# Kernel tuning notes

Hardware: AMD Instinct MI355X
Metric: run time of the kernel (lower is better)

## Reference

```python
import jax, jax.numpy as jnp
import numpy as np

N_NODES = 100000
N_EDGES = 1600000


def _spmm(row, col, val, x, n):
    # out[i] = sum_{e: row[e]==i} val[e] * x[col[e]]  (sparse adj @ dense x)
    return jax.ops.segment_sum(val[:, None] * x[col], row, num_segments=n)


def setup_inputs() -> dict:
    key = jax.random.key(0)
    ks = jax.random.split(key, 6)
    x = jax.random.normal(ks[0], (N_NODES, 128), dtype=jnp.float32)
    edge_row = jnp.sort(jax.random.randint(ks[1], (N_EDGES,), 0, N_NODES, dtype=jnp.int64))
    edge_col = jax.random.randint(ks[2], (N_EDGES,), 0, N_NODES, dtype=jnp.int64)
    # glorot-initialized linear layers (pyg Linear with weight_initializer='glorot')
    W0 = jax.random.normal(ks[3], (128, 128), dtype=jnp.float32) * np.sqrt(2.0 / (128 + 128))
    b0 = jnp.zeros((128,), dtype=jnp.float32)
    W1 = jax.random.normal(ks[4], (128, 64), dtype=jnp.float32) * np.sqrt(2.0 / (128 + 64))
    b1 = jnp.zeros((64,), dtype=jnp.float32)
    return {"x": x, "edge_row": edge_row, "edge_col": edge_col,
            "W0": W0, "b0": b0, "W1": W1, "b1": b1}


def reference(x, edge_row, edge_col, W0, b0, W1, b1):
    n = x.shape[0]
    # adj_norm: symmetric GCN normalization D^{-1/2} A D^{-1/2}
    ones = jnp.ones(edge_row.shape[0], dtype=x.dtype)
    deg = jax.ops.segment_sum(ones, edge_row, num_segments=n)
    dinv = jnp.where(deg > 0, jax.lax.rsqrt(jnp.maximum(deg, 1.0)), 0.0).astype(x.dtype)
    val = dinv[edge_row] * dinv[edge_col]
    # layer 0: linear -> SpMM -> relu (dropout is a no-op in inference/eval)
    h = x @ W0 + b0
    h = _spmm(edge_row, edge_col, val, h, n)
    h = jax.nn.relu(h)
    # layer 1: linear -> SpMM
    h = h @ W1 + b1
    h = _spmm(edge_row, edge_col, val, h, n)
    return jax.nn.log_softmax(h, axis=-1)
```

## Files before the change

### kernel.cpp

```cpp
#include <hip/hip_runtime.h>
#include <hip/hip_bf16.h>

#define NN 100000
#define NE 1600000

typedef __bf16 bf16x8 __attribute__((ext_vector_type(8)));
typedef float  f32x4  __attribute__((ext_vector_type(4)));

__device__ inline int rfl(int x) { return __builtin_amdgcn_readfirstlane(x); }

__device__ inline void acc2(float& a, float& b, unsigned int u) {
    a += __uint_as_float(u << 16);
    b += __uint_as_float(u & 0xffff0000u);
}

__device__ inline unsigned int pack_bf2(float x, float y) {
    union { __hip_bfloat162 h; unsigned int u; } p;
    p.h = __float22bfloat162_rn(make_float2(x, y));
    return p.u;
}

__global__ __launch_bounds__(256) void prep_kernel(const int* __restrict__ row,
                                                   int* __restrict__ row_ptr,
                                                   const float* __restrict__ W0,
                                                   const float* __restrict__ W1,
                                                   __hip_bfloat16* __restrict__ Wt0,
                                                   __hip_bfloat16* __restrict__ Wt1) {
    int b = blockIdx.x;
    if (b < NE / 256) {
        int e = b * 256 + threadIdx.x;
        int r  = row[e];
        int rp = (e == 0) ? -1 : row[e - 1];
        for (int i = rp + 1; i <= r; ++i) row_ptr[i] = e;
        if (e == NE - 1) {
            for (int i = r + 1; i <= NN; ++i) row_ptr[i] = NE;
        }
    } else {
        int idx = (b - NE / 256) * 256 + threadIdx.x;
        if (idx < 128 * 128) {
            int n = idx >> 7, k = idx & 127;
            Wt0[idx] = __float2bfloat16(W0[(size_t)k * 128 + n]);
        } else {
            int r2 = idx - 128 * 128;
            int n = r2 >> 7, k = r2 & 127;
            Wt1[r2] = __float2bfloat16(W1[(size_t)k * 64 + n]);
        }
    }
}

__device__ inline float deg_scale(const int* __restrict__ row_ptr, int i) {
    int dg = row_ptr[i + 1] - row_ptr[i];
    return (dg > 0) ? rsqrtf((float)dg) : 0.0f;
}

template <int NO, typename InT>
__global__ __launch_bounds__(512) void gemm_mfma(const InT* __restrict__ X,
                                                 const __hip_bfloat16* __restrict__ Wt,
                                                 const float* __restrict__ bias,
                                                 const int* __restrict__ row_ptr,
                                                 __hip_bfloat16* __restrict__ out, int M) {
    constexpr int NT = NO / 16;
    __shared__ unsigned short SH[128 * 128];

    const int t = threadIdx.x;
    const int w = t >> 6, lane = t & 63;
    const int l15 = lane & 15, quad = lane >> 4;
    const int rbase = blockIdx.x * 128;

    for (int i = t; i < NO * 16; i += 512) {
        int n = i >> 4, g = i & 15;
        *(uint4*)&SH[n * 128 + ((g ^ (n & 7)) << 3)] = ((const uint4*)Wt)[i];
    }
    __syncthreads();

    const int arow_g = rbase + w * 16 + l15;
    const int arow   = (arow_g < M) ? arow_g : (M - 1);

    bf16x8 af[4];
    if constexpr (sizeof(InT) == 4) {
        float4 lo[4], hi[4];
#pragma unroll
        for (int kc = 0; kc < 4; ++kc) {
            const float4* src = (const float4*)&X[(size_t)arow * 128 + kc * 32 + quad * 8];
            lo[kc] = src[0];
            hi[kc] = src[1];
        }
#pragma unroll
        for (int kc = 0; kc < 4; ++kc) {
            union { bf16x8 v; __hip_bfloat162 h[4]; } u;
            u.h[0] = __float22bfloat162_rn(make_float2(lo[kc].x, lo[kc].y));
            u.h[1] = __float22bfloat162_rn(make_float2(lo[kc].z, lo[kc].w));
            u.h[2] = __float22bfloat162_rn(make_float2(hi[kc].x, hi[kc].y));
            u.h[3] = __float22bfloat162_rn(make_float2(hi[kc].z, hi[kc].w));
            af[kc] = u.v;
        }
    } else {
        union { bf16x8 v; uint4 q; } u[4];
#pragma unroll
        for (int kc = 0; kc < 4; ++kc)
            u[kc].q = *(const uint4*)&X[(size_t)arow * 128 + kc * 32 + quad * 8];
#pragma unroll
        for (int kc = 0; kc < 4; ++kc) af[kc] = u[kc].v;
    }

    f32x4 acc[NT];
#pragma unroll
    for (int nt = 0; nt < NT; ++nt) {
        float bv = bias[nt * 16 + l15];
        acc[nt][0] = bv; acc[nt][1] = bv; acc[nt][2] = bv; acc[nt][3] = bv;
    }

#pragma unroll
    for (int kc = 0; kc < 4; ++kc) {
#pragma unroll
        for (int nt = 0; nt < NT; ++nt) {
            int brow = nt * 16 + l15;
            bf16x8 bfr = *(const bf16x8*)&SH[brow * 128 + (((kc * 4 + quad) ^ (brow & 7)) << 3)];
            acc[nt] = __builtin_amdgcn_mfma_f32_16x16x32_bf16(af[kc], bfr, acc[nt], 0, 0, 0);
        }
    }
    __syncthreads();

    __hip_bfloat16* Cp = (__hip_bfloat16*)SH;
#pragma unroll
    for (int r4 = 0; r4 < 4; ++r4) {
        int lrow = w * 16 + quad * 4 + r4;
        int grow = rbase + lrow;
        float sc = (grow < M) ? deg_scale(row_ptr, grow) : 0.f;
#pragma unroll
        for (int nt = 0; nt < NT; ++nt) {
            int ct = nt * 16 + l15;
            Cp[lrow * 128 + ((((ct >> 3) ^ (lrow & 7)) << 3)) + (ct & 7)] =
                __float2bfloat16(acc[nt][r4] * sc);
        }
    }
    constexpr int RJ  = NO / 8;
    constexpr int CNT = (16 * RJ) / 64;
#pragma unroll
    for (int k = 0; k < CNT; ++k) {
        int idx = k * 64 + lane;
        int lr16 = idx / RJ, j = idx % RJ;
        int lrow = w * 16 + lr16;
        int grow = rbase + lrow;
        if (grow < M) {
            uint4 v = *(const uint4*)&Cp[lrow * 128 + ((j ^ (lrow & 7)) << 3)];
            *(uint4*)&out[(size_t)grow * NO + (j << 3)] = v;
        }
    }
}

__global__ __launch_bounds__(512) void spmm_relu_gemm1(const int* __restrict__ row_ptr,
                                                       const int* __restrict__ col,
                                                       const uint4* __restrict__ H4,
                                                       const __hip_bfloat16* __restrict__ Wt1,
                                                       const float* __restrict__ b1,
                                                       __hip_bfloat16* __restrict__ out) {
    __shared__ unsigned short As[32 * 128];
    __shared__ unsigned short Ws[64 * 128];

    const int t = threadIdx.x;
    const int w = t >> 6, lane = t & 63;
    const int l15 = lane & 15, quad = lane >> 4;
    const int rbase = blockIdx.x * 32;
    const int p = lane >> 4;
    const int q = lane & 15;

    for (int i = t; i < 64 * 16; i += 512) {
        int n = i >> 4, g = i & 15;
        *(uint4*)&Ws[n * 128 + ((g ^ (n & 7)) << 3)] = ((const uint4*)Wt1)[i];
    }

#pragma unroll 1
    for (int rr = 0; rr < 4; ++rr) {
        const int il = w * 4 + rr;
        const int i  = rbase + il;
        const int e0 = rfl(row_ptr[i]);
        const int e1 = rfl(row_ptr[i + 1]);
        const int dg = e1 - e0;
        const float di = (dg > 0) ? rsqrtf((float)dg) : 0.0f;
        float a0 = 0.f, a1 = 0.f, a2 = 0.f, a3 = 0.f,
              a4 = 0.f, a5 = 0.f, a6 = 0.f, a7 = 0.f;

        if (dg > 0) {
            const int em    = e1 - 1;
            const int nfull = dg >> 4;
            const int tb    = e0 + (nfull << 4);
            const bool tail = (dg & 15) != 0;
            uint4 va[4], vb[4];

            auto ISSUEF = [&](uint4* v, int base) {
#pragma unroll
                for (int g2 = 0; g2 < 4; ++g2) {
                    int eb = base + g2 * 4;
                    int s0 = rfl(col[eb]), s1 = rfl(col[eb + 1]);
                    int s2 = rfl(col[eb + 2]), s3 = rfl(col[eb + 3]);
                    int c01 = (p & 1) ? s1 : s0;
                    int c23 = (p & 1) ? s3 : s2;
                    int c   = (p & 2) ? c23 : c01;
                    v[g2] = H4[(size_t)c * 16 + q];
                }
            };
            auto ISSUET = [&](uint4* v) {
#pragma unroll
                for (int g2 = 0; g2 < 4; ++g2) {
                    int eb = tb + g2 * 4;
                    int j0 = (eb     > em) ? em : eb;
                    int j1 = (eb + 1 > em) ? em : eb + 1;
                    int j2 = (eb + 2 > em) ? em : eb + 2;
                    int j3 = (eb + 3 > em) ? em : eb + 3;
                    int s0 = rfl(col[j0]), s1 = rfl(col[j1]);
                    int s2 = rfl(col[j2]), s3 = rfl(col[j3]);
                    int c01 = (p & 1) ? s1 : s0;
                    int c23 = (p & 1) ? s3 : s2;
                    int c   = (p & 2) ? c23 : c01;
                    v[g2] = H4[(size_t)c * 16 + q];
                }
            };
            auto CONSF = [&](const uint4* v) {
#pragma unroll
                for (int g2 = 0; g2 < 4; ++g2) {
                    acc2(a0, a1, v[g2].x); acc2(a2, a3, v[g2].y);
                    acc2(a4, a5, v[g2].z); acc2(a6, a7, v[g2].w);
                }
            };
            auto CONST_ = [&](const uint4* v) {
#pragma unroll
                for (int g2 = 0; g2 < 4; ++g2) {
                    uint4 u = v[g2];
                    if (tb + g2 * 4 + p >= e1) { u.x = 0u; u.y = 0u; u.z = 0u; u.w = 0u; }
                    acc2(a0, a1, u.x); acc2(a2, a3, u.y);
                    acc2(a4, a5, u.z); acc2(a6, a7, u.w);
                }
            };

            if (nfull > 0) {
                ISSUEF(va, e0);
                int b = 1;
#pragma unroll 1
                for (; b + 1 < nfull; b += 2) {
                    ISSUEF(vb, e0 + 16 * b);
                    CONSF(va);
                    ISSUEF(va, e0 + 16 * (b + 1));
                    CONSF(vb);
                }
                if (b < nfull) {
                    ISSUEF(vb, e0 + 16 * b);
                    CONSF(va);
                    if (tail) { ISSUET(va); CONSF(vb); CONST_(va); }
                    else      { CONSF(vb); }
                } else {
                    if (tail) { ISSUET(vb); CONSF(va); CONST_(vb); }
                    else      { CONSF(va); }
                }
            } else {
                ISSUET(va);
                CONST_(va);
            }
        }

#pragma unroll
        for (int off = 16; off < 64; off <<= 1) {
            a0 += __shfl_xor(a0, off, 64); a1 += __shfl_xor(a1, off, 64);
            a2 += __shfl_xor(a2, off, 64); a3 += __shfl_xor(a3, off, 64);
            a4 += __shfl_xor(a4, off, 64); a5 += __shfl_xor(a5, off, 64);
            a6 += __shfl_xor(a6, off, 64); a7 += __shfl_xor(a7, off, 64);
        }
        if (p == 0) {
            uint4 pk;
            pk.x = pack_bf2(fmaxf(a0 * di, 0.f), fmaxf(a1 * di, 0.f));
            pk.y = pack_bf2(fmaxf(a2 * di, 0.f), fmaxf(a3 * di, 0.f));
            pk.z = pack_bf2(fmaxf(a4 * di, 0.f), fmaxf(a5 * di, 0.f));
            pk.w = pack_bf2(fmaxf(a6 * di, 0.f), fmaxf(a7 * di, 0.f));
            *(uint4*)&As[il * 128 + ((q ^ (il & 7)) << 3)] = pk;
        }
    }
    __syncthreads();

    const int rb = (w & 1) * 16;
    const int cb = (w >> 1) * 16;
    const int arow_l = rb + l15;
    const int asw = arow_l & 7;

    f32x4 acc;
    {
        float bv = b1[cb + l15];
        acc[0] = bv; acc[1] = bv; acc[2] = bv; acc[3] = bv;
    }
#pragma unroll
    for (int kc = 0; kc < 4; ++kc) {
        bf16x8 af = *(const bf16x8*)&As[arow_l * 128 + (((kc * 4 + quad) ^ asw) << 3)];
        int brow = cb + l15;
        bf16x8 bfr = *(const bf16x8*)&Ws[brow * 128 + (((kc * 4 + quad) ^ (brow & 7)) << 3)];
        acc = __builtin_amdgcn_mfma_f32_16x16x32_bf16(af, bfr, acc, 0, 0, 0);
    }

#pragma unroll
    for (int r4 = 0; r4 < 4; ++r4) {
        int grow = rbase + rb + quad * 4 + r4;
        float sc = deg_scale(row_ptr, grow);
        out[(size_t)grow * 64 + cb + l15] = __float2bfloat16(acc[r4] * sc);
    }
}

__global__ __launch_bounds__(256) void spmm_logsoftmax_64(const int* __restrict__ row_ptr,
                                                          const int* __restrict__ col,
                                                          const uint4* __restrict__ H4,
                                                          float* __restrict__ out, int N) {
    const int lane = threadIdx.x & 63;
    const int p = lane >> 3;
    const int q = lane & 7;
    int i = rfl(blockIdx.x * 4 + (threadIdx.x >> 6));
    if (i >= N) return;
    const int e0 = rfl(row_ptr[i]);
    const int e1 = rfl(row_ptr[i + 1]);
    const int dg = e1 - e0;
    const float di = (dg > 0) ? rsqrtf((float)dg) : 0.0f;
    float a0 = 0.f, a1 = 0.f, a2 = 0.f, a3 = 0.f,
          a4 = 0.f, a5 = 0.f, a6 = 0.f, a7 = 0.f;

    if (dg > 0) {
        const int em    = e1 - 1;
        const int nfull = dg >> 3;
        const int tb    = e0 + (nfull << 3);
        const bool tail = (dg & 7) != 0;
        uint4 ua, ub;

        auto PICK = [&](int s0, int s1, int s2, int s3,
                        int s4, int s5, int s6, int s7) {
            int b0 = (p & 1) ? s1 : s0, b1_ = (p & 1) ? s3 : s2;
            int b2 = (p & 1) ? s5 : s4, b3_ = (p & 1) ? s7 : s6;
            int c0 = (p & 2) ? b1_ : b0, c1 = (p & 2) ? b3_ : b2;
            return (p & 4) ? c1 : c0;
        };
        auto ISSUEF = [&](uint4& u, int base) {
            int c = PICK(rfl(col[base]),     rfl(col[base + 1]),
                         rfl(col[base + 2]), rfl(col[base + 3]),
                         rfl(col[base + 4]), rfl(col[base + 5]),
                         rfl(col[base + 6]), rfl(col[base + 7]));
            u = H4[(size_t)c * 8 + q];
        };
        auto ISSUET = [&](uint4& u) {
            int j0 = tb,     j1 = tb + 1, j2 = tb + 2, j3 = tb + 3;
            int j4 = tb + 4, j5 = tb + 5, j6 = tb + 6, j7 = tb + 7;
            j1 = (j1 > em) ? em : j1; j2 = (j2 > em) ? em : j2;
            j3 = (j3 > em) ? em : j3; j4 = (j4 > em) ? em : j4;
            j5 = (j5 > em) ? em : j5; j6 = (j6 > em) ? em : j6;
            j7 = (j7 > em) ? em : j7;
            int c = PICK(rfl(col[j0]), rfl(col[j1]), rfl(col[j2]), rfl(col[j3]),
                         rfl(col[j4]), rfl(col[j5]), rfl(col[j6]), rfl(col[j7]));
            u = H4[(size_t)c * 8 + q];
        };
        auto CONSF = [&](uint4 u) {
            acc2(a0, a1, u.x); acc2(a2, a3, u.y);
            acc2(a4, a5, u.z); acc2(a6, a7, u.w);
        };
        auto CONST_ = [&](uint4 u) {
            if (tb + p >= e1) { u.x = 0u; u.y = 0u; u.z = 0u; u.w = 0u; }
            acc2(a0, a1, u.x); acc2(a2, a3, u.y);
            acc2(a4, a5, u.z); acc2(a6, a7, u.w);
        };

        if (nfull > 0) {
            ISSUEF(ua, e0);
            int g = 1;
#pragma unroll 1
            for (; g + 1 < nfull; g += 2) {
                ISSUEF(ub, e0 + 8 * g);
                CONSF(ua);
                ISSUEF(ua, e0 + 8 * (g + 1));
                CONSF(ub);
            }
            if (g < nfull) {
                ISSUEF(ub, e0 + 8 * g);
                CONSF(ua);
                if (tail) { ISSUET(ua); CONSF(ub); CONST_(ua); }
                else      { CONSF(ub); }
            } else {
                if (tail) { ISSUET(ub); CONSF(ua); CONST_(ub); }
                else      { CONSF(ua); }
            }
        } else {
            ISSUET(ua);
            CONST_(ua);
        }
    }

#pragma unroll
    for (int off = 8; off < 64; off <<= 1) {
        a0 += __shfl_xor(a0, off, 64); a1 += __shfl_xor(a1, off, 64);
        a2 += __shfl_xor(a2, off, 64); a3 += __shfl_xor(a3, off, 64);
        a4 += __shfl_xor(a4, off, 64); a5 += __shfl_xor(a5, off, 64);
        a6 += __shfl_xor(a6, off, 64); a7 += __shfl_xor(a7, off, 64);
    }
    a0 *= di; a1 *= di; a2 *= di; a3 *= di;
    a4 *= di; a5 *= di; a6 *= di; a7 *= di;
    float m = fmaxf(fmaxf(fmaxf(a0, a1), fmaxf(a2, a3)),
                    fmaxf(fmaxf(a4, a5), fmaxf(a6, a7)));
#pragma unroll
    for (int off = 1; off < 8; off <<= 1)
        m = fmaxf(m, __shfl_xor(m, off, 64));
    float s = __expf(a0 - m) + __expf(a1 - m) + __expf(a2 - m) + __expf(a3 - m)
            + __expf(a4 - m) + __expf(a5 - m) + __expf(a6 - m) + __expf(a7 - m);
#pragma unroll
    for (int off = 1; off < 8; off <<= 1)
        s += __shfl_xor(s, off, 64);
    float ls = __logf(s);
    if (p == 0) {
        float4 o0 = make_float4(a0 - m - ls, a1 - m - ls, a2 - m - ls, a3 - m - ls);
        float4 o1 = make_float4(a4 - m - ls, a5 - m - ls, a6 - m - ls, a7 - m - ls);
        *(float4*)&out[(size_t)i * 64 + q * 8]     = o0;
        *(float4*)&out[(size_t)i * 64 + q * 8 + 4] = o1;
    }
}

extern "C" void kernel_launch(void* const* d_in, const int* in_sizes, int n_in,
                              void* d_out, int out_size, void* d_ws, size_t ws_size,
                              hipStream_t stream) {
    const float* x    = (const float*)d_in[0];
    const int*   erow = (const int*)d_in[1];
    const int*   ecol = (const int*)d_in[2];
    const float* W0   = (const float*)d_in[3];
    const float* b0   = (const float*)d_in[4];
    const float* W1   = (const float*)d_in[5];
    const float* b1   = (const float*)d_in[6];
    float* out = (float*)d_out;

    char* ws = (char*)d_ws;
    int*             row_ptr = (int*)ws;
    __hip_bfloat16*  h0b     = (__hip_bfloat16*)(ws + (1u << 20));
    __hip_bfloat16*  h2b     = (__hip_bfloat16*)(ws + 27000000u);
    __hip_bfloat16*  Wt0     = (__hip_bfloat16*)(ws + 41000000u);
    __hip_bfloat16*  Wt1     = (__hip_bfloat16*)(ws + 41100000u);

    prep_kernel<<<NE / 256 + 96, 256, 0, stream>>>(erow, row_ptr, W0, W1, Wt0, Wt1);
    gemm_mfma<128, float><<<(NN + 127) / 128, 512, 0, stream>>>(x, Wt0, b0, row_ptr, h0b, NN);
    spmm_relu_gemm1<<<NN / 32, 512, 0, stream>>>(row_ptr, ecol,
                                                 (const uint4*)h0b, Wt1, b1, h2b);
    spmm_logsoftmax_64<<<(NN + 3) / 4, 256, 0, stream>>>(row_ptr, ecol,
                                                         (const uint4*)h2b, out, NN);
}
```

Before: 225.4 us.

## Process two rows per wave in final SpMM with four-deep gather pipeline

The final SpMM+log_softmax kernel now assigns two consecutive rows to each wavefront and merges their edge chunks into one stream. Four gather loads are kept in flight instead of two. Column indices are now loaded per lane rather than as eight scalar readfirstlane loads with a select tree. This is meant to raise memory-level parallelism and amortize per-row setup, at the cost of more registers, per-chunk branching between the two rows, and half as many waves.

```diff
diff --git a/kernel.cpp b/kernel.cpp
--- a/kernel.cpp
+++ b/kernel.cpp
@@ -309,108 +309,98 @@
     const int lane = threadIdx.x & 63;
     const int p = lane >> 3;
     const int q = lane & 7;
-    int i = rfl(blockIdx.x * 4 + (threadIdx.x >> 6));
-    if (i >= N) return;
-    const int e0 = rfl(row_ptr[i]);
-    const int e1 = rfl(row_ptr[i + 1]);
-    const int dg = e1 - e0;
-    const float di = (dg > 0) ? rsqrtf((float)dg) : 0.0f;
-    float a0 = 0.f, a1 = 0.f, a2 = 0.f, a3 = 0.f,
-          a4 = 0.f, a5 = 0.f, a6 = 0.f, a7 = 0.f;
-
-    if (dg > 0) {
-        const int em    = e1 - 1;
-        const int nfull = dg >> 3;
-        const int tb    = e0 + (nfull << 3);
-        const bool tail = (dg & 7) != 0;
-        uint4 ua, ub;
-
-        auto PICK = [&](int s0, int s1, int s2, int s3,
-                        int s4, int s5, int s6, int s7) {
-            int b0 = (p & 1) ? s1 : s0, b1_ = (p & 1) ? s3 : s2;
-            int b2 = (p & 1) ? s5 : s4, b3_ = (p & 1) ? s7 : s6;
-            int c0 = (p & 2) ? b1_ : b0, c1 = (p & 2) ? b3_ : b2;
-            return (p & 4) ? c1 : c0;
-        };
-        auto ISSUEF = [&](uint4& u, int base) {
-            int c = PICK(rfl(col[base]),     rfl(col[base + 1]),
-                         rfl(col[base + 2]), rfl(col[base + 3]),
-                         rfl(col[base + 4]), rfl(col[base + 5]),
-                         rfl(col[base + 6]), rfl(col[base + 7]));
-            u = H4[(size_t)c * 8 + q];
-        };
-        auto ISSUET = [&](uint4& u) {
-            int j0 = tb,     j1 = tb + 1, j2 = tb + 2, j3 = tb + 3;
-            int j4 = tb + 4, j5 = tb + 5, j6 = tb + 6, j7 = tb + 7;
-            j1 = (j1 > em) ? em : j1; j2 = (j2 > em) ? em : j2;
-            j3 = (j3 > em) ? em : j3; j4 = (j4 > em) ? em : j4;
-            j5 = (j5 > em) ? em : j5; j6 = (j6 > em) ? em : j6;
-            j7 = (j7 > em) ? em : j7;
-            int c = PICK(rfl(col[j0]), rfl(col[j1]), rfl(col[j2]), rfl(col[j3]),
-                         rfl(col[j4]), rfl(col[j5]), rfl(col[j6]), rfl(col[j7]));
-            u = H4[(size_t)c * 8 + q];
-        };
-        auto CONSF = [&](uint4 u) {
-            acc2(a0, a1, u.x); acc2(a2, a3, u.y);
-            acc2(a4, a5, u.z); acc2(a6, a7, u.w);
-        };
-        auto CONST_ = [&](uint4 u) {
-            if (tb + p >= e1) { u.x = 0u; u.y = 0u; u.z = 0u; u.w = 0u; }
-            acc2(a0, a1, u.x); acc2(a2, a3, u.y);
-            acc2(a4, a5, u.z); acc2(a6, a7, u.w);
-        };
-
-        if (nfull > 0) {
-            ISSUEF(ua, e0);
-            int g = 1;
+    const int iA = rfl(blockIdx.x * 8 + (threadIdx.x >> 6) * 2);
+    if (iA >= N) return;
+    const int e0A = rfl(row_ptr[iA]);
+    const int e1A = rfl(row_ptr[iA + 1]);
+    const int e1B = rfl(row_ptr[iA + 2]);
+    const int e0B = e1A;
+    const int dgA = e1A - e0A, dgB = e1B - e0B;
+    const int nA = (dgA + 7) >> 3;
+    const int nB = (dgB + 7) >> 3;
+    const int NT = nA + nB;
+
+    float aA[8] = {0.f, 0.f, 0.f, 0.f, 0.f, 0.f, 0.f, 0.f};
+    float aB[8] = {0.f, 0.f, 0.f, 0.f, 0.f, 0.f, 0.f, 0.f};
+
+    auto ISSUE = [&](uint4& u, int j) {
+        int base, em;
+        if (j < nA) { base = e0A + (j << 3);        em = e1A - 1; }
+        else        { base = e0B + ((j - nA) << 3); em = e1B - 1; }
+        int e = base + p;
+        e = (e > em) ? em : e;
+        int c = col[e];
+        u = H4[(size_t)c * 8 + q];
+    };
+    auto ACC8 = [&](uint4 u, float (&a)[8]) {
+        acc2(a[0], a[1], u.x); acc2(a[2], a[3], u.y);
+        acc2(a[4], a[5], u.z); acc2(a[6], a[7], u.w);
+    };
+    auto CONSUME = [&](uint4 u, int j) {
+        if (j < nA) {
+            if ((j == nA - 1) && (dgA & 7)) {
+                if (e0A + (j << 3) + p >= e1A) { u.x = 0u; u.y = 0u; u.z = 0u; u.w = 0u; }
+            }
+            ACC8(u, aA);
+        } else {
+            if ((j == NT - 1) && (dgB & 7)) {
+                if (e0B + ((j - nA) << 3) + p >= e1B) { u.x = 0u; u.y = 0u; u.z = 0u; u.w = 0u; }
+            }
+            ACC8(u, aB);
+        }
+    };
+
+    if (NT > 0) {
+        uint4 u0, u1, u2, u3;
+        ISSUE(u0, 0);
+        if (NT > 1) ISSUE(u1, 1);
+        if (NT > 2) ISSUE(u2, 2);
+        if (NT > 3) ISSUE(u3, 3);
+        int j = 0;
 #pragma unroll 1
-            for (; g + 1 < nfull; g += 2) {
-                ISSUEF(ub, e0 + 8 * g);
-                CONSF(ua);
-                ISSUEF(ua, e0 + 8 * (g + 1));
-                CONSF(ub);
-            }
-            if (g < nfull) {
-                ISSUEF(ub, e0 + 8 * g);
-                CONSF(ua);
-                if (tail) { ISSUET(ua); CONSF(ub); CONST_(ua); }
-                else      { CONSF(ub); }
-            } else {
-                if (tail) { ISSUET(ub); CONSF(ua); CONST_(ub); }
-                else      { CONSF(ua); }
-            }
-        } else {
-            ISSUET(ua);
-            CONST_(ua);
-        }
-    }
-
-#pragma unroll
-    for (int off = 8; off < 64; off <<= 1) {
-        a0 += __shfl_xor(a0, off, 64); a1 += __shfl_xor(a1, off, 64);
-        a2 += __shfl_xor(a2, off, 64); a3 += __shfl_xor(a3, off, 64);
-        a4 += __shfl_xor(a4, off, 64); a5 += __shfl_xor(a5, off, 64);
-        a6 += __shfl_xor(a6, off, 64); a7 += __shfl_xor(a7, off, 64);
-    }
-    a0 *= di; a1 *= di; a2 *= di; a3 *= di;
-    a4 *= di; a5 *= di; a6 *= di; a7 *= di;
-    float m = fmaxf(fmaxf(fmaxf(a0, a1), fmaxf(a2, a3)),
-                    fmaxf(fmaxf(a4, a5), fmaxf(a6, a7)));
-#pragma unroll
-    for (int off = 1; off < 8; off <<= 1)
-        m = fmaxf(m, __shfl_xor(m, off, 64));
-    float s = __expf(a0 - m) + __expf(a1 - m) + __expf(a2 - m) + __expf(a3 - m)
-            + __expf(a4 - m) + __expf(a5 - m) + __expf(a6 - m) + __expf(a7 - m);
-#pragma unroll
-    for (int off = 1; off < 8; off <<= 1)
-        s += __shfl_xor(s, off, 64);
-    float ls = __logf(s);
-    if (p == 0) {
-        float4 o0 = make_float4(a0 - m - ls, a1 - m - ls, a2 - m - ls, a3 - m - ls);
-        float4 o1 = make_float4(a4 - m - ls, a5 - m - ls, a6 - m - ls, a7 - m - ls);
-        *(float4*)&out[(size_t)i * 64 + q * 8]     = o0;
-        *(float4*)&out[(size_t)i * 64 + q * 8 + 4] = o1;
-    }
+        for (; j + 4 < NT; j += 4) {
+            CONSUME(u0, j);     ISSUE(u0, j + 4);
+            CONSUME(u1, j + 1); if (j + 5 < NT) ISSUE(u1, j + 5);
+            CONSUME(u2, j + 2); if (j + 6 < NT) ISSUE(u2, j + 6);
+            CONSUME(u3, j + 3); if (j + 7 < NT) ISSUE(u3, j + 7);
+        }
+        CONSUME(u0, j);
+        if (j + 1 < NT) CONSUME(u1, j + 1);
+        if (j + 2 < NT) CONSUME(u2, j + 2);
+        if (j + 3 < NT) CONSUME(u3, j + 3);
+    }
+
+    auto FINISH = [&](int i, float (&a)[8], int dg) {
+        const float di = (dg > 0) ? rsqrtf((float)dg) : 0.0f;
+#pragma unroll
+        for (int off = 8; off < 64; off <<= 1) {
+#pragma unroll
+            for (int r = 0; r < 8; ++r) a[r] += __shfl_xor(a[r], off, 64);
+        }
+#pragma unroll
+        for (int r = 0; r < 8; ++r) a[r] *= di;
+        float m = a[0];
+#pragma unroll
+        for (int r = 1; r < 8; ++r) m = fmaxf(m, a[r]);
+#pragma unroll
+        for (int off = 1; off < 8; off <<= 1)
+            m = fmaxf(m, __shfl_xor(m, off, 64));
+        float s = 0.f;
+#pragma unroll
+        for (int r = 0; r < 8; ++r) s += __expf(a[r] - m);
+#pragma unroll
+        for (int off = 1; off < 8; off <<= 1)
+            s += __shfl_xor(s, off, 64);
+        float ls = __logf(s) + m;
+        if (p == 0) {
+            float4 o0 = make_float4(a[0] - ls, a[1] - ls, a[2] - ls, a[3] - ls);
+            float4 o1 = make_float4(a[4] - ls, a[5] - ls, a[6] - ls, a[7] - ls);
+            *(float4*)&out[(size_t)i * 64 + q * 8]     = o0;
+            *(float4*)&out[(size_t)i * 64 + q * 8 + 4] = o1;
+        }
+    };
+    FINISH(iA,     aA, dgA);
+    FINISH(iA + 1, aB, dgB);
 }
 
 extern "C" void kernel_launch(void* const* d_in, const int* in_sizes, int n_in,
@@ -436,6 +426,6 @@
     gemm_mfma<128, float><<<(NN + 127) / 128, 512, 0, stream>>>(x, Wt0, b0, row_ptr, h0b, NN);
     spmm_relu_gemm1<<<NN / 32, 512, 0, stream>>>(row_ptr, ecol,
                                                  (const uint4*)h0b, Wt1, b1, h2b);
-    spmm_logsoftmax_64<<<(NN + 3) / 4, 256, 0, stream>>>(row_ptr, ecol,
+    spmm_logsoftmax_64<<<(NN + 7) / 8, 256, 0, stream>>>(row_ptr, ecol,
                                                          (const uint4*)h2b, out, NN);
 }
```

Result: slower. 354.0 us (+57.0%).
